# Kernel optimization log

Hardware: AMD Instinct MI355X
Metric: run time of the kernel (lower is better)

## Reference

```python
import jax, jax.numpy as jnp
import numpy as np

B = 131072       # batch rows
IN_DIM = 256     # in_dim
N_BINS = 128     # n_bins
N_KNOTS = 8      # n_knots
OUT_DIM = 3 * (N_KNOTS + 1)  # 27


def setup_inputs() -> dict:
    key = jax.random.key(0)
    k1, k2, k3 = jax.random.split(key, 3)
    h = jax.random.normal(k1, (B, IN_DIM), dtype=jnp.float32)
    W = jax.random.normal(k2, (OUT_DIM, IN_DIM), dtype=jnp.float32) / np.sqrt(IN_DIM).astype(np.float32)
    b = jax.random.normal(k3, (OUT_DIM,), dtype=jnp.float32) * 0.01
    return {"h": h, "W": W, "b": b}


def _rqs(x, cumx, cumy, d):
    # x: [B, n_bins+1]; cumx, cumy: [B, n_knots+2]; d: [B, n_knots+3]
    widths = cumx[..., 1:] - cumx[..., :-1]    # [B, K+1]
    heights = cumy[..., 1:] - cumy[..., :-1]   # [B, K+1]
    delta = heights / widths
    # torch.searchsorted(right=False) == jnp.searchsorted(side='left'), batched per row
    bin_idx = jax.vmap(lambda a, v: jnp.searchsorted(a, v, side='left'))(cumx[..., 1:], x)
    bin_idx = jnp.minimum(bin_idx, widths.shape[-1] - 1)
    gather = lambda t: jnp.take_along_axis(t, bin_idx, axis=-1)
    in_cumx = gather(cumx)
    in_cumy = gather(cumy)
    in_w = gather(widths)
    in_h = gather(heights)
    in_delta = gather(delta)
    in_d = gather(d)
    in_d1 = jnp.take_along_axis(d, bin_idx + 1, axis=-1)
    theta = (x - in_cumx) / in_w
    t1m = theta * (1.0 - theta)
    numerator = in_h * (in_delta * theta * theta + in_d * t1m)
    denominator = in_delta + (in_d + in_d1 - 2.0 * in_delta) * t1m
    return in_cumy + numerator / denominator


def reference(h, W, b):
    params = jax.nn.softplus(h @ W.T + b) + 1e-4   # [B, 3*(K+1)]
    K1 = N_KNOTS + 1
    w = params[:, :K1]
    hh = params[:, K1:2 * K1]
    d = params[:, 2 * K1:]
    w = w / jnp.sum(w, axis=-1, keepdims=True)
    hh = hh / jnp.sum(hh, axis=-1, keepdims=True)
    cumx = jnp.pad(jnp.cumsum(w, axis=-1), ((0, 0), (1, 0)))   # [B, K+2]
    cumy = jnp.pad(jnp.cumsum(hh, axis=-1), ((0, 0), (1, 0)))  # [B, K+2]
    d = jnp.pad(d, ((0, 0), (1, 1)), constant_values=1.0)      # [B, K+3]
    edges = jnp.linspace(0.0, 1.0, N_BINS + 1, dtype=h.dtype)
    x = jnp.broadcast_to(edges, (h.shape[0], N_BINS + 1))
    F_edges = _rqs(x, cumx, cumy, d)                            # [B, n_bins+1]
    probs = F_edges[:, 1:] - F_edges[:, :-1]
    return jnp.log(jnp.clip(probs, 1e-8))
```

## Files before the change

### kernel.cpp

```cpp
#include <hip/hip_runtime.h>
#include <cstdint>
#include <math.h>

#define IN_DIM 256
#define OUT_DIM 27
#define NK1 9

__device__ __forceinline__ double fast_rcp(double d) {
    double r = (double)__builtin_amdgcn_rcpf((float)d);
    r = r * (2.0 - d * r);
    r = r * (2.0 - d * r);
    return r;
}

__global__ __launch_bounds__(256, 4)
void gemv_params3(const float* __restrict__ h, const float* __restrict__ W,
                  const float* __restrict__ bias, float* __restrict__ paramsT,
                  int nrows)
{
    __shared__ float wlds[IN_DIM * 28];
    const int t = threadIdx.x;
    const int w = t >> 6, l = t & 63;
    const size_t row0 = (size_t)blockIdx.x * 64;

#pragma unroll
    for (int nn = 0; nn < OUT_DIM; ++nn)
        wlds[t * 28 + nn] = W[nn * IN_DIM + t];
    wlds[t * 28 + 27] = 0.f;
    __syncthreads();

    float4 hreg[16];
    const float* hbase = h + (row0 + l) * IN_DIM + w * 64;
#pragma unroll
    for (int j = 0; j < 16; ++j)
        hreg[j] = *reinterpret_cast<const float4*>(hbase + j * 4);

    float acc[28];
#pragma unroll
    for (int i = 0; i < 28; ++i) acc[i] = 0.f;

#pragma unroll
    for (int j = 0; j < 16; ++j) {
        const float4 hv4 = hreg[j];
#pragma unroll
        for (int kk = 0; kk < 4; ++kk) {
            const float hv = (kk == 0) ? hv4.x : (kk == 1) ? hv4.y
                           : (kk == 2) ? hv4.z : hv4.w;
            const float* wr = &wlds[(w * 64 + j * 4 + kk) * 28];
#pragma unroll
            for (int q = 0; q < 7; ++q) {
                const float4 wq = *reinterpret_cast<const float4*>(wr + q * 4);
                acc[q * 4 + 0] = fmaf(hv, wq.x, acc[q * 4 + 0]);
                acc[q * 4 + 1] = fmaf(hv, wq.y, acc[q * 4 + 1]);
                acc[q * 4 + 2] = fmaf(hv, wq.z, acc[q * 4 + 2]);
                acc[q * 4 + 3] = fmaf(hv, wq.w, acc[q * 4 + 3]);
            }
        }
    }

    __syncthreads();
#pragma unroll
    for (int nn = 0; nn < OUT_DIM; ++nn)
        wlds[t * 28 + nn] = acc[nn];
    __syncthreads();

    const int row = t & 63, grp = t >> 6;
    const int nn0 = grp * 7;
    const int nnE = (nn0 + 7 < OUT_DIM) ? nn0 + 7 : OUT_DIM;
    for (int nn = nn0; nn < nnE; ++nn) {
        const float s = wlds[(0 * 64 + row) * 28 + nn] + wlds[(1 * 64 + row) * 28 + nn]
                      + wlds[(2 * 64 + row) * 28 + nn] + wlds[(3 * 64 + row) * 28 + nn];
        const float x  = s + bias[nn];
        const float sp = fmaxf(x, 0.f) + log1pf(expf(-fabsf(x))) + 1e-4f;
        paramsT[(size_t)nn * nrows + row0 + row] = sp;
    }
}

__global__ __launch_bounds__(256)
void spline_eval3(const float* __restrict__ paramsT, float* __restrict__ out,
                  int nrows)
{
    __shared__ float  sp[4][27];
    __shared__ double cxs[4][10];
    __shared__ double cf[4][9][9];
    const int t = threadIdx.x;
    const size_t r0 = (size_t)blockIdx.x * 4;

    if (t < 108) {
        const int j = t >> 2, r = t & 3;
        sp[r][j] = paramsT[(size_t)j * nrows + r0 + r];
    }
    __syncthreads();
    if (t < 4) {
        const int r = t;
        double ws = 0.0, hs = 0.0;
#pragma unroll
        for (int i = 0; i < NK1; ++i) { ws += (double)sp[r][i]; hs += (double)sp[r][NK1 + i]; }
        const double iws = fast_rcp(ws), ihs = fast_rcp(hs);
        double cumx[10], cumy[10];
        cumx[0] = 0.0; cumy[0] = 0.0;
#pragma unroll
        for (int i = 0; i < NK1; ++i) {
            cumx[i + 1] = cumx[i] + (double)sp[r][i] * iws;
            cumy[i + 1] = cumy[i] + (double)sp[r][NK1 + i] * ihs;
        }
#pragma unroll
        for (int b = 0; b < 9; ++b) {
            const double db  = (b == 0) ? 1.0 : (double)sp[r][2 * NK1 + b - 1];
            const double db1 = (double)sp[r][2 * NK1 + b];
            const double wb  = cumx[b + 1] - cumx[b];
            const double hb  = cumy[b + 1] - cumy[b];
            const double iw  = fast_rcp(wb);
            const double dl  = hb * iw;
            cf[r][b][0] = cumx[b];
            cf[r][b][1] = cumy[b];
            cf[r][b][2] = iw;
            cf[r][b][3] = dl;
            cf[r][b][4] = hb;
            cf[r][b][5] = db;
            cf[r][b][6] = db + db1 - 2.0 * dl;
            cxs[r][b]   = cumx[b];
        }
        cxs[r][9] = cumx[9];
    }
    __syncthreads();

    const int r  = t >> 6;
    const int lq = t & 63;

    double cx_[9];
#pragma unroll
    for (int i = 0; i < 9; ++i) cx_[i] = cxs[r][i + 1];

    auto evalF = [&](double x) -> double {
        int b = 0;
#pragma unroll
        for (int i = 0; i < 9; ++i) b += (cx_[i] < x) ? 1 : 0;
        b = (b < 8) ? b : 8;
        const double* c = cf[r][b];
        const double th  = (x - c[0]) * c[2];
        const double t1m = th * (1.0 - th);
        const double num = c[4] * (c[3] * th * th + c[5] * t1m);
        const double den = c[3] + c[6] * t1m;
        return c[1] + num * fast_rcp(den);
    };

    const double x0 = (double)(lq * 2) * 0.0078125;
    const double F0 = evalF(x0);
    const double F1 = evalF(x0 + 0.0078125);
    double F2 = __shfl_down(F0, 1);
    if (lq == 63) F2 = evalF(1.0);
    const float p0 = __logf(fmaxf((float)(F1 - F0), 1e-8f));
    const float p1 = __logf(fmaxf((float)(F2 - F1), 1e-8f));
    *reinterpret_cast<float2*>(out + (r0 + r) * 128 + lq * 2) = make_float2(p0, p1);
}

__device__ __forceinline__ double softplus_d(double x) {
    return fmax(x, 0.0) + log1p(exp(-fabs(x)));
}

__global__ __launch_bounds__(256)
void rqs_head_fallback(const float* __restrict__ h, const float* __restrict__ Wmat,
                       const float* __restrict__ b, float* __restrict__ out) {
    __shared__ float sh[128][33];
    const int t = threadIdx.x, rl = t >> 1, half = t & 1;
    const long row0 = (long)blockIdx.x * 128;
    float acc[OUT_DIM];
#pragma unroll
    for (int i = 0; i < OUT_DIM; ++i) acc[i] = 0.0f;
    for (int kc = 0; kc < 8; ++kc) {
        __syncthreads();
#pragma unroll
        for (int p = 0; p < 4; ++p) {
            const int r = p * 32 + (t / 8), fq = t % 8;
            const float4 v = *reinterpret_cast<const float4*>(
                &h[(row0 + r) * IN_DIM + (size_t)kc * 32 + fq * 4]);
            sh[r][fq*4+0]=v.x; sh[r][fq*4+1]=v.y; sh[r][fq*4+2]=v.z; sh[r][fq*4+3]=v.w;
        }
        __syncthreads();
#pragma unroll
        for (int kk = 0; kk < 16; ++kk) {
            const int kl = half * 16 + kk;
            const float hv = sh[rl][kl];
            const int kg = kc * 32 + kl;
#pragma unroll
            for (int nn = 0; nn < OUT_DIM; ++nn)
                acc[nn] = fmaf(hv, Wmat[nn * IN_DIM + kg], acc[nn]);
        }
    }
#pragma unroll
    for (int nn = 0; nn < OUT_DIM; ++nn) acc[nn] += __shfl_xor(acc[nn], 1);
    double pr[OUT_DIM];
#pragma unroll
    for (int nn = 0; nn < OUT_DIM; ++nn)
        pr[nn] = softplus_d((double)acc[nn] + (double)b[nn]) + 1e-4;
    double wsum = 0.0, hsum = 0.0;
#pragma unroll
    for (int i = 0; i < NK1; ++i) { wsum += pr[i]; hsum += pr[NK1 + i]; }
    const double iws = 1.0 / wsum, ihs = 1.0 / hsum;
    double cumx[NK1+1], cumy[NK1+1], dfull[NK1+1];
    cumx[0]=0.0; cumy[0]=0.0; dfull[0]=1.0;
#pragma unroll
    for (int i = 0; i < NK1; ++i) {
        cumx[i+1] = cumx[i] + pr[i]*iws;
        cumy[i+1] = cumy[i] + pr[NK1+i]*ihs;
        dfull[i+1] = pr[2*NK1+i];
    }
    const int e0 = half * 64, eend = e0 + 64;
    int e = e0; double prevF = 0.0;
    float* orow = out + (row0 + rl) * 128;
#define BIN_BODY(bin_) { \
    const double cx=cumx[bin_], cxn=((bin_)<8)?cumx[(bin_)+1]:1.0e300, cy=cumy[bin_]; \
    const double wb=cumx[(bin_)+1]-cx, hb=cumy[(bin_)+1]-cy; \
    const double iw=1.0/wb, dl=hb*iw, db=dfull[bin_], db1=dfull[(bin_)+1]; \
    const double sc=db+db1-2.0*dl; \
    while (e <= eend) { \
        const double x=(double)e*0.0078125; \
        if (x > cxn) break; \
        const double th=(x-cx)*iw, t1m=th*(1.0-th); \
        const double num=hb*(dl*th*th+db*t1m), den=dl+sc*t1m; \
        const double F=cy+num/den; \
        if (e > e0) orow[e-1] = logf(fmaxf((float)(F-prevF), 1e-8f)); \
        prevF=F; ++e; \
    } }
    BIN_BODY(0) BIN_BODY(1) BIN_BODY(2) BIN_BODY(3) BIN_BODY(4)
    BIN_BODY(5) BIN_BODY(6) BIN_BODY(7) BIN_BODY(8)
#undef BIN_BODY
}

extern "C" void kernel_launch(void* const* d_in, const int* in_sizes, int n_in,
                              void* d_out, int out_size, void* d_ws, size_t ws_size,
                              hipStream_t stream) {
    const float* h = (const float*)d_in[0];
    const float* W = (const float*)d_in[1];
    const float* b = (const float*)d_in[2];
    float* out = (float*)d_out;

    const int rows = in_sizes[0] / IN_DIM;
    const size_t need = (size_t)OUT_DIM * rows * sizeof(float);

    if (ws_size >= need) {
        float* paramsT = (float*)d_ws;
        gemv_params3 <<<rows / 64, 256, 0, stream>>>(h, W, b, paramsT, rows);
        spline_eval3 <<<rows / 4,  256, 0, stream>>>(paramsT, out, rows);
    } else {
        rqs_head_fallback<<<rows / 128, 256, 0, stream>>>(h, W, b, out);
    }
}
```

Before: 301.1 us.

## Restructure GEMV staging and spline coefficient setup with row-major params

The GEMV kernel now gives each wave its own 64-row slice of W in LDS and stages h in coalesced, padded LDS chunks split into two halves, so the global load of the second half overlaps the FMAs on the first. Params are written row-major with a stride of 28 instead of transposed. The spline kernel has each wave load its own row directly, compute the nine bin coefficients in parallel across lanes, and sync with a wave barrier instead of block barriers. Bin search now compares in float, the reciprocal refinement drops to one Newton step, and the final edge value is taken as exactly 1.0. The float bin search and single Newton step could change results slightly near knot boundaries.

```diff
diff --git a/kernel.cpp b/kernel.cpp
--- a/kernel.cpp
+++ b/kernel.cpp
@@ -5,154 +5,188 @@
 #define IN_DIM 256
 #define OUT_DIM 27
 #define NK1 9
-
-__device__ __forceinline__ double fast_rcp(double d) {
+#define PST 28
+
+__device__ __forceinline__ double fast_rcp2(double d) {
     double r = (double)__builtin_amdgcn_rcpf((float)d);
     r = r * (2.0 - d * r);
     r = r * (2.0 - d * r);
     return r;
 }
-
-__global__ __launch_bounds__(256, 4)
-void gemv_params3(const float* __restrict__ h, const float* __restrict__ W,
-                  const float* __restrict__ bias, float* __restrict__ paramsT,
-                  int nrows)
+__device__ __forceinline__ double fast_rcp1(double d) {
+    double r = (double)__builtin_amdgcn_rcpf((float)d);
+    r = r * (2.0 - d * r);
+    return r;
+}
+
+__global__ __launch_bounds__(256)
+void gemv_params4(const float* __restrict__ h, const float* __restrict__ W,
+                  const float* __restrict__ bias, float* __restrict__ params)
 {
-    __shared__ float wlds[IN_DIM * 28];
+    __shared__ float wq[4][64 * 28];
+    __shared__ float hc[4][64 * 36];
     const int t = threadIdx.x;
     const int w = t >> 6, l = t & 63;
     const size_t row0 = (size_t)blockIdx.x * 64;
 
+    float* wl = wq[w];
+    float* hw = hc[w];
+    const float* hbase = h + row0 * IN_DIM + w * 64;
+
+    float wtmp[OUT_DIM];
 #pragma unroll
     for (int nn = 0; nn < OUT_DIM; ++nn)
-        wlds[t * 28 + nn] = W[nn * IN_DIM + t];
-    wlds[t * 28 + 27] = 0.f;
+        wtmp[nn] = W[nn * IN_DIM + w * 64 + l];
+
+    float4 st[8];
+#pragma unroll
+    for (int i = 0; i < 8; ++i) {
+        const int f = i * 64 + l;
+        st[i] = *reinterpret_cast<const float4*>(
+            hbase + (f >> 3) * IN_DIM + (f & 7) * 4);
+    }
+
+#pragma unroll
+    for (int nn = 0; nn < OUT_DIM; ++nn) wl[l * 28 + nn] = wtmp[nn];
+    wl[l * 28 + 27] = 0.f;
+
+#pragma unroll
+    for (int i = 0; i < 8; ++i) {
+        const int f = i * 64 + l;
+        *reinterpret_cast<float4*>(hw + ((f >> 3) * 9 + (f & 7)) * 4) = st[i];
+    }
+
+#pragma unroll
+    for (int i = 0; i < 8; ++i) {
+        const int f = i * 64 + l;
+        st[i] = *reinterpret_cast<const float4*>(
+            hbase + (f >> 3) * IN_DIM + 32 + (f & 7) * 4);
+    }
+
+    float acc[28];
+#pragma unroll
+    for (int i = 0; i < 28; ++i) acc[i] = 0.f;
+
+#define FMA_CHUNK(koff_)                                                      \
+    _Pragma("unroll")                                                         \
+    for (int c4 = 0; c4 < 8; ++c4) {                                          \
+        const float4 hv4 = *reinterpret_cast<const float4*>(                  \
+            hw + (l * 9 + c4) * 4);                                           \
+        _Pragma("unroll")                                                     \
+        for (int kk = 0; kk < 4; ++kk) {                                      \
+            const float hv = (kk == 0) ? hv4.x : (kk == 1) ? hv4.y            \
+                           : (kk == 2) ? hv4.z : hv4.w;                       \
+            const float* wr = wl + ((koff_) + c4 * 4 + kk) * 28;              \
+            _Pragma("unroll")                                                 \
+            for (int q = 0; q < 7; ++q) {                                     \
+                const float4 wv = *reinterpret_cast<const float4*>(wr + q*4); \
+                acc[q*4+0] = fmaf(hv, wv.x, acc[q*4+0]);                      \
+                acc[q*4+1] = fmaf(hv, wv.y, acc[q*4+1]);                      \
+                acc[q*4+2] = fmaf(hv, wv.z, acc[q*4+2]);                      \
+                acc[q*4+3] = fmaf(hv, wv.w, acc[q*4+3]);                      \
+            }                                                                 \
+        }                                                                     \
+    }
+
+    FMA_CHUNK(0)
+
+#pragma unroll
+    for (int i = 0; i < 8; ++i) {
+        const int f = i * 64 + l;
+        *reinterpret_cast<float4*>(hw + ((f >> 3) * 9 + (f & 7)) * 4) = st[i];
+    }
+
+    FMA_CHUNK(32)
+#undef FMA_CHUNK
+
     __syncthreads();
-
-    float4 hreg[16];
-    const float* hbase = h + (row0 + l) * IN_DIM + w * 64;
-#pragma unroll
-    for (int j = 0; j < 16; ++j)
-        hreg[j] = *reinterpret_cast<const float4*>(hbase + j * 4);
-
-    float acc[28];
-#pragma unroll
-    for (int i = 0; i < 28; ++i) acc[i] = 0.f;
-
-#pragma unroll
-    for (int j = 0; j < 16; ++j) {
-        const float4 hv4 = hreg[j];
-#pragma unroll
-        for (int kk = 0; kk < 4; ++kk) {
-            const float hv = (kk == 0) ? hv4.x : (kk == 1) ? hv4.y
-                           : (kk == 2) ? hv4.z : hv4.w;
-            const float* wr = &wlds[(w * 64 + j * 4 + kk) * 28];
-#pragma unroll
-            for (int q = 0; q < 7; ++q) {
-                const float4 wq = *reinterpret_cast<const float4*>(wr + q * 4);
-                acc[q * 4 + 0] = fmaf(hv, wq.x, acc[q * 4 + 0]);
-                acc[q * 4 + 1] = fmaf(hv, wq.y, acc[q * 4 + 1]);
-                acc[q * 4 + 2] = fmaf(hv, wq.z, acc[q * 4 + 2]);
-                acc[q * 4 + 3] = fmaf(hv, wq.w, acc[q * 4 + 3]);
-            }
+#pragma unroll
+    for (int nn = 0; nn < OUT_DIM; ++nn) hc[w][l * 28 + nn] = acc[nn];
+    __syncthreads();
+
+    const int row = t & 63, grp = t >> 6;
+#pragma unroll
+    for (int j = 0; j < 7; ++j) {
+        const int nn = grp * 7 + j;
+        if (nn < OUT_DIM) {
+            const float s = hc[0][row * 28 + nn] + hc[1][row * 28 + nn]
+                          + hc[2][row * 28 + nn] + hc[3][row * 28 + nn];
+            const float x  = s + bias[nn];
+            const float sp = fmaxf(x, 0.f) + log1pf(expf(-fabsf(x))) + 1e-4f;
+            params[(row0 + row) * PST + nn] = sp;
         }
     }
-
-    __syncthreads();
-#pragma unroll
-    for (int nn = 0; nn < OUT_DIM; ++nn)
-        wlds[t * 28 + nn] = acc[nn];
-    __syncthreads();
-
-    const int row = t & 63, grp = t >> 6;
-    const int nn0 = grp * 7;
-    const int nnE = (nn0 + 7 < OUT_DIM) ? nn0 + 7 : OUT_DIM;
-    for (int nn = nn0; nn < nnE; ++nn) {
-        const float s = wlds[(0 * 64 + row) * 28 + nn] + wlds[(1 * 64 + row) * 28 + nn]
-                      + wlds[(2 * 64 + row) * 28 + nn] + wlds[(3 * 64 + row) * 28 + nn];
-        const float x  = s + bias[nn];
-        const float sp = fmaxf(x, 0.f) + log1pf(expf(-fabsf(x))) + 1e-4f;
-        paramsT[(size_t)nn * nrows + row0 + row] = sp;
-    }
 }
 
 __global__ __launch_bounds__(256)
-void spline_eval3(const float* __restrict__ paramsT, float* __restrict__ out,
-                  int nrows)
+void spline_eval4(const float* __restrict__ params, float* __restrict__ out)
 {
-    __shared__ float  sp[4][27];
-    __shared__ double cxs[4][10];
     __shared__ double cf[4][9][9];
     const int t = threadIdx.x;
-    const size_t r0 = (size_t)blockIdx.x * 4;
-
-    if (t < 108) {
-        const int j = t >> 2, r = t & 3;
-        sp[r][j] = paramsT[(size_t)j * nrows + r0 + r];
-    }
-    __syncthreads();
-    if (t < 4) {
-        const int r = t;
+    const int r = t >> 6, lq = t & 63;
+    const int row = __builtin_amdgcn_readfirstlane((int)(blockIdx.x * 4 + r));
+
+    const float* prow = params + (size_t)row * PST;
+    float p[OUT_DIM];
+#pragma unroll
+    for (int j = 0; j < OUT_DIM; ++j) p[j] = prow[j];
+
+    float wsf = 0.f;
+#pragma unroll
+    for (int i = 0; i < 9; ++i) wsf += p[i];
+    const float iwf = 1.0f / wsf;
+    float cumf[9];
+    {
+        float s = 0.f;
+#pragma unroll
+        for (int i = 0; i < 9; ++i) { s += p[i]; cumf[i] = s * iwf; }
+    }
+
+    if (lq < 9) {
+        const int b = lq;
         double ws = 0.0, hs = 0.0;
 #pragma unroll
-        for (int i = 0; i < NK1; ++i) { ws += (double)sp[r][i]; hs += (double)sp[r][NK1 + i]; }
-        const double iws = fast_rcp(ws), ihs = fast_rcp(hs);
-        double cumx[10], cumy[10];
-        cumx[0] = 0.0; cumy[0] = 0.0;
-#pragma unroll
-        for (int i = 0; i < NK1; ++i) {
-            cumx[i + 1] = cumx[i] + (double)sp[r][i] * iws;
-            cumy[i + 1] = cumy[i] + (double)sp[r][NK1 + i] * ihs;
-        }
-#pragma unroll
-        for (int b = 0; b < 9; ++b) {
-            const double db  = (b == 0) ? 1.0 : (double)sp[r][2 * NK1 + b - 1];
-            const double db1 = (double)sp[r][2 * NK1 + b];
-            const double wb  = cumx[b + 1] - cumx[b];
-            const double hb  = cumy[b + 1] - cumy[b];
-            const double iw  = fast_rcp(wb);
-            const double dl  = hb * iw;
-            cf[r][b][0] = cumx[b];
-            cf[r][b][1] = cumy[b];
-            cf[r][b][2] = iw;
-            cf[r][b][3] = dl;
-            cf[r][b][4] = hb;
-            cf[r][b][5] = db;
-            cf[r][b][6] = db + db1 - 2.0 * dl;
-            cxs[r][b]   = cumx[b];
-        }
-        cxs[r][9] = cumx[9];
-    }
-    __syncthreads();
-
-    const int r  = t >> 6;
-    const int lq = t & 63;
-
-    double cx_[9];
-#pragma unroll
-    for (int i = 0; i < 9; ++i) cx_[i] = cxs[r][i + 1];
-
-    auto evalF = [&](double x) -> double {
+        for (int i = 0; i < 9; ++i) { ws += (double)p[i]; hs += (double)p[9 + i]; }
+        const double iws = fast_rcp2(ws), ihs = fast_rcp2(hs);
+        double pw = 0.0, ph = 0.0;
+        for (int i = 0; i < b; ++i) { pw += (double)p[i]; ph += (double)p[9 + i]; }
+        const double cx  = pw * iws;
+        const double cy  = ph * ihs;
+        const double wb  = (double)p[b] * iws;
+        const double hb  = (double)p[9 + b] * ihs;
+        const double iw  = fast_rcp2(wb);
+        const double dl  = hb * iw;
+        const double db  = (b == 0) ? 1.0 : (double)p[17 + b];
+        const double db1 = (double)p[18 + b];
+        cf[r][b][0] = cx;  cf[r][b][1] = cy;  cf[r][b][2] = iw;
+        cf[r][b][3] = dl;  cf[r][b][4] = hb;  cf[r][b][5] = db;
+        cf[r][b][6] = db + db1 - 2.0 * dl;
+    }
+    __builtin_amdgcn_wave_barrier();
+
+    auto evalF = [&](double x, float xf) -> double {
         int b = 0;
 #pragma unroll
-        for (int i = 0; i < 9; ++i) b += (cx_[i] < x) ? 1 : 0;
+        for (int i = 0; i < 9; ++i) b += (cumf[i] < xf) ? 1 : 0;
         b = (b < 8) ? b : 8;
         const double* c = cf[r][b];
         const double th  = (x - c[0]) * c[2];
         const double t1m = th * (1.0 - th);
         const double num = c[4] * (c[3] * th * th + c[5] * t1m);
         const double den = c[3] + c[6] * t1m;
-        return c[1] + num * fast_rcp(den);
+        return c[1] + num * fast_rcp1(den);
     };
 
-    const double x0 = (double)(lq * 2) * 0.0078125;
-    const double F0 = evalF(x0);
-    const double F1 = evalF(x0 + 0.0078125);
-    double F2 = __shfl_down(F0, 1);
-    if (lq == 63) F2 = evalF(1.0);
+    const double x0 = (double)lq * (1.0 / 64.0);
+    const double x1 = x0 + (1.0 / 128.0);
+    const double F0 = evalF(x0, (float)lq * (1.0f / 64.0f));
+    const double F1 = evalF(x1, (float)(2 * lq + 1) * (1.0f / 128.0f));
+    const double Fn = __shfl_down(F0, 1);
+    const double F2 = (lq == 63) ? 1.0 : Fn;
+
     const float p0 = __logf(fmaxf((float)(F1 - F0), 1e-8f));
     const float p1 = __logf(fmaxf((float)(F2 - F1), 1e-8f));
-    *reinterpret_cast<float2*>(out + (r0 + r) * 128 + lq * 2) = make_float2(p0, p1);
+    *reinterpret_cast<float2*>(out + (size_t)row * 128 + lq * 2) = make_float2(p0, p1);
 }
 
 __device__ __forceinline__ double softplus_d(double x) {
@@ -237,12 +271,12 @@
     float* out = (float*)d_out;
 
     const int rows = in_sizes[0] / IN_DIM;
-    const size_t need = (size_t)OUT_DIM * rows * sizeof(float);
+    const size_t need = (size_t)rows * PST * sizeof(float);
 
     if (ws_size >= need) {
-        float* paramsT = (float*)d_ws;
-        gemv_params3 <<<rows / 64, 256, 0, stream>>>(h, W, b, paramsT, rows);
-        spline_eval3 <<<rows / 4,  256, 0, stream>>>(paramsT, out, rows);
+        float* params = (float*)d_ws;
+        gemv_params4 <<<rows / 64, 256, 0, stream>>>(h, W, b, params);
+        spline_eval4 <<<rows / 4,  256, 0, stream>>>(params, out);
     } else {
         rqs_head_fallback<<<rows / 128, 256, 0, stream>>>(h, W, b, out);
     }
```

New measurement: 368.5 us. +22.4%, slower.
